# Optimization experiments

Measured on AMD Instinct MI355X. Metric: run time of the kernel, lower is better.

The kernel has to match this reference:

```python
import jax, jax.numpy as jnp
import numpy as np

B, S, VDIM, EDIM, K = 8, 2048, 1024, 256, 8192


def setup_inputs() -> dict:
    key = jax.random.key(0)
    k1, k2, k3, k4 = jax.random.split(key, 4)
    values = jax.random.normal(k1, (B, S, VDIM), dtype=jnp.float32)
    # nn.Linear(value_dim, embed_dim): weight [EDIM, VDIM], bias [EDIM]
    lim = 1.0 / np.sqrt(VDIM)
    W = jax.random.uniform(k2, (EDIM, VDIM), dtype=jnp.float32, minval=-lim, maxval=lim)
    b = jax.random.uniform(k3, (EDIM,), dtype=jnp.float32, minval=-lim, maxval=lim)
    # nn.Embedding default init: N(0, 1)
    codebook = jax.random.normal(k4, (K, EDIM), dtype=jnp.float32)
    return {"values": values, "W": W, "b": b, "codebook": codebook}


def reference(values, W, b, codebook):
    # Linear projection: [B,S,VDIM] -> [B,S,EDIM]
    projected = jnp.einsum("bsv,ev->bse", values, W) + b
    flat = projected.reshape(-1, projected.shape[-1])  # [N, EDIM]
    # Squared Euclidean distances via expansion (argmin-equivalent to cdist)
    d2 = (
        jnp.sum(flat * flat, axis=-1, keepdims=True)
        - 2.0 * (flat @ codebook.T)
        + jnp.sum(codebook * codebook, axis=-1)
    )  # [N, K]
    phase_ids = jnp.argmin(d2, axis=-1).reshape(values.shape[:-1])  # [B, S]
    quantized = codebook[phase_ids]  # [B, S, EDIM]
    sg = jax.lax.stop_gradient
    commitment_loss = jnp.mean((projected - sg(quantized)) ** 2)
    codebook_loss = jnp.mean((sg(projected) - quantized) ** 2)
    vq_loss = codebook_loss + 0.25 * commitment_loss
    # straight-through estimator
    quantized_st = projected + sg(quantized - projected)
    return quantized_st, phase_ids, vq_loss
```

## Files before the change

kernel.cpp:

```cpp
#include <hip/hip_runtime.h>

typedef __attribute__((ext_vector_type(8))) short bf16x8;
typedef __attribute__((ext_vector_type(4))) float f32x4;
typedef unsigned int uint32;
typedef unsigned long long ull;

#define NR 16384
#define VD 1024
#define ED 256
#define KC 8192
#define NBUCK 16
#define DELTA 2.0f
#define VSHIFT 128.0f

__device__ __forceinline__ uint32 f2u(float f){ return __float_as_uint(f); }
__device__ __forceinline__ float u2f(uint32 u){ return __uint_as_float(u); }

__device__ __forceinline__ uint32 pkbf(float lo, float hi){
  uint32 a = __float_as_uint(lo); a += 0x7fffu + ((a >> 16) & 1u);
  uint32 b = __float_as_uint(hi); b += 0x7fffu + ((b >> 16) & 1u);
  return (a >> 16) | (b & 0xffff0000u);
}

#define GLOAD_LDS16(g, l) __builtin_amdgcn_global_load_lds( \
    (const __attribute__((address_space(1))) void*)(g),     \
    (__attribute__((address_space(3))) void*)(l), 16, 0, 0)
#define GLOAD_LDS4(g, l) __builtin_amdgcn_global_load_lds(  \
    (const __attribute__((address_space(1))) void*)(g),     \
    (__attribute__((address_space(3))) void*)(l), 4, 0, 0)

__global__ __launch_bounds__(256) void wconv_kernel(
    const float* __restrict__ W, ushort* __restrict__ Whi, ushort* __restrict__ Wlo)
{
  const int idx = (blockIdx.x * 256 + threadIdx.x) * 8;
  float4 a = *(const float4*)(W + idx);
  float4 b = *(const float4*)(W + idx + 4);
  uint32 h01 = (f2u(a.x) >> 16) | (f2u(a.y) & 0xffff0000u);
  uint32 h23 = (f2u(a.z) >> 16) | (f2u(a.w) & 0xffff0000u);
  uint32 h45 = (f2u(b.x) >> 16) | (f2u(b.y) & 0xffff0000u);
  uint32 h67 = (f2u(b.z) >> 16) | (f2u(b.w) & 0xffff0000u);
  float r0 = a.x - u2f(f2u(a.x) & 0xffff0000u);
  float r1 = a.y - u2f(f2u(a.y) & 0xffff0000u);
  float r2 = a.z - u2f(f2u(a.z) & 0xffff0000u);
  float r3 = a.w - u2f(f2u(a.w) & 0xffff0000u);
  float r4 = b.x - u2f(f2u(b.x) & 0xffff0000u);
  float r5 = b.y - u2f(f2u(b.y) & 0xffff0000u);
  float r6 = b.z - u2f(f2u(b.z) & 0xffff0000u);
  float r7 = b.w - u2f(f2u(b.w) & 0xffff0000u);
  *(uint4*)(Whi + idx) = make_uint4(h01, h23, h45, h67);
  *(uint4*)(Wlo + idx) = make_uint4(pkbf(r0,r1), pkbf(r2,r3), pkbf(r4,r5), pkbf(r6,r7));
}

__global__ __launch_bounds__(512) void proj_mfma(
    const float* __restrict__ V, const ushort* __restrict__ WhiG,
    const ushort* __restrict__ WloG, const float* __restrict__ bias,
    float* __restrict__ C, ushort* __restrict__ Pbf)
{
  __shared__ __align__(16) char lds[128 * 132 * 4];
  const int rowbase = blockIdx.x * 128;
  const int colbase = blockIdx.y * 128;
  const int t = threadIdx.x, l = t & 63, w = t >> 6;
  const int c0 = l & 15, g = l >> 4;
  const int rg = w >> 2, cg = w & 3;

  const int srow = t >> 2, sq = t & 3;
  const float* aSrc = V + (size_t)(rowbase + srow) * VD + sq * 8;
  const int wu0 = (sq - (srow >> 3)) & 3;
  const ushort* whSrc = WhiG + (size_t)(colbase + srow) * VD + wu0 * 8;
  const ushort* wlSrc = WloG + (size_t)(colbase + srow) * VD + wu0 * 8;
  const int awOff = srow * 64 + (((sq + (srow >> 3)) & 3) << 4);
  char* wdst = lds + 16384 + (size_t)w * 1024;

  float4 bv[2];
  bv[0] = *(const float4*)&bias[colbase + cg * 32 + g * 4];
  bv[1] = *(const float4*)&bias[colbase + cg * 32 + 16 + g * 4];

  int vOff[4], wOff[2];
  #pragma unroll
  for (int bi = 0; bi < 4; ++bi) {
    int r = rg * 64 + bi * 16 + c0;
    vOff[bi] = r * 64 + (((g + (r >> 3)) & 3) << 4);
  }
  #pragma unroll
  for (int aj = 0; aj < 2; ++aj) {
    int r = cg * 32 + aj * 16 + c0;
    wOff[aj] = r * 64 + (((g + (r >> 3)) & 3) << 4);
  }

  f32x4 acc[2][4];
  #pragma unroll
  for (int aj = 0; aj < 2; ++aj)
    #pragma unroll
    for (int bi = 0; bi < 4; ++bi) acc[aj][bi] = (f32x4){0.f,0.f,0.f,0.f};

  float4 fa0, fa1;
  #define LOAD_A(ch)  { fa0 = *(const float4*)(aSrc + (ch) * 32); \
                        fa1 = *(const float4*)(aSrc + (ch) * 32 + 4); }
  #define STAGE_W(ch, buf) { \
    GLOAD_LDS16(whSrc + (ch) * 32, wdst + (buf) * 32768);        \
    GLOAD_LDS16(wlSrc + (ch) * 32, wdst + (buf) * 32768 + 8192); }
  #define CONV_WRITE(buf) { \
    uint32 h01 = (f2u(fa0.x)>>16)|(f2u(fa0.y)&0xffff0000u); \
    uint32 h23 = (f2u(fa0.z)>>16)|(f2u(fa0.w)&0xffff0000u); \
    uint32 h45 = (f2u(fa1.x)>>16)|(f2u(fa1.y)&0xffff0000u); \
    uint32 h67 = (f2u(fa1.z)>>16)|(f2u(fa1.w)&0xffff0000u); \
    float r0 = fa0.x - u2f(f2u(fa0.x)&0xffff0000u); \
    float r1 = fa0.y - u2f(f2u(fa0.y)&0xffff0000u); \
    float r2 = fa0.z - u2f(f2u(fa0.z)&0xffff0000u); \
    float r3 = fa0.w - u2f(f2u(fa0.w)&0xffff0000u); \
    float r4 = fa1.x - u2f(f2u(fa1.x)&0xffff0000u); \
    float r5 = fa1.y - u2f(f2u(fa1.y)&0xffff0000u); \
    float r6 = fa1.z - u2f(f2u(fa1.z)&0xffff0000u); \
    float r7 = fa1.w - u2f(f2u(fa1.w)&0xffff0000u); \
    *(uint4*)(lds + (buf)*32768 + awOff) = make_uint4(h01,h23,h45,h67); \
    *(uint4*)(lds + (buf)*32768 + 8192 + awOff) = \
        make_uint4(pkbf(r0,r1), pkbf(r2,r3), pkbf(r4,r5), pkbf(r6,r7)); }
  #define COMPUTE(buf) { \
    const char* Bq = lds + (buf) * 32768; \
    bf16x8 vh[4], vl[4], wh[2], wl[2]; \
    _Pragma("unroll") \
    for (int bi = 0; bi < 4; ++bi) { \
      vh[bi] = *(const bf16x8*)(Bq + vOff[bi]); \
      vl[bi] = *(const bf16x8*)(Bq + 8192 + vOff[bi]); } \
    _Pragma("unroll") \
    for (int aj = 0; aj < 2; ++aj) { \
      wh[aj] = *(const bf16x8*)(Bq + 16384 + wOff[aj]); \
      wl[aj] = *(const bf16x8*)(Bq + 24576 + wOff[aj]); } \
    _Pragma("unroll") \
    for (int aj = 0; aj < 2; ++aj) \
      _Pragma("unroll") \
      for (int bi = 0; bi < 4; ++bi) { \
        acc[aj][bi] = __builtin_amdgcn_mfma_f32_16x16x32_bf16(wh[aj], vh[bi], acc[aj][bi], 0, 0, 0); \
        acc[aj][bi] = __builtin_amdgcn_mfma_f32_16x16x32_bf16(wh[aj], vl[bi], acc[aj][bi], 0, 0, 0); \
        acc[aj][bi] = __builtin_amdgcn_mfma_f32_16x16x32_bf16(wl[aj], vh[bi], acc[aj][bi], 0, 0, 0); } }

  LOAD_A(0); STAGE_W(0, 0);
  CONV_WRITE(0);
  __syncthreads();
  int buf = 0;
  for (int ch = 0; ch < 32; ++ch) {
    if (ch < 31) { LOAD_A(ch + 1); STAGE_W(ch + 1, buf ^ 1); }
    COMPUTE(buf);
    if (ch < 31) CONV_WRITE(buf ^ 1);
    __syncthreads();
    buf ^= 1;
  }
  #undef LOAD_A
  #undef STAGE_W
  #undef CONV_WRITE
  #undef COMPUTE

  float* Cs = (float*)lds;
  #pragma unroll
  for (int aj = 0; aj < 2; ++aj)
    #pragma unroll
    for (int bi = 0; bi < 4; ++bi) {
      int prow = rg * 64 + bi * 16 + c0;
      int pcol = cg * 32 + aj * 16 + g * 4;
      f32x4 v = acc[aj][bi];
      float4 o = make_float4(v[0] + bv[aj].x, v[1] + bv[aj].y,
                             v[2] + bv[aj].z, v[3] + bv[aj].w);
      *(float4*)&Cs[prow * 132 + pcol] = o;
    }
  __syncthreads();
  {
    const int row = t >> 2, qd = t & 3;
    const float* src = &Cs[row * 132 + qd * 32];
    float* cdst = &C[(size_t)(rowbase + row) * ED + colbase + qd * 32];
    float4 vv[8];
    #pragma unroll
    for (int i = 0; i < 8; ++i) vv[i] = *(const float4*)(src + i * 4);
    #pragma unroll
    for (int i = 0; i < 8; ++i) *(float4*)(cdst + i * 4) = vv[i];
    uint4 pk[4];
    #pragma unroll
    for (int i = 0; i < 4; ++i)
      pk[i] = make_uint4(pkbf(vv[2*i].x, vv[2*i].y), pkbf(vv[2*i].z, vv[2*i].w),
                         pkbf(vv[2*i+1].x, vv[2*i+1].y), pkbf(vv[2*i+1].z, vv[2*i+1].w));
    uint4* pdst = (uint4*)&Pbf[(size_t)(rowbase + row) * ED + colbase + qd * 32];
    #pragma unroll
    for (int i = 0; i < 4; ++i) pdst[i] = pk[i];
  }
}

__global__ __launch_bounds__(256) void cnormbf_kernel(
    const float* __restrict__ CB, float* __restrict__ cnorm,
    float* __restrict__ cnAdj, ushort* __restrict__ CBbf)
{
  const int t = threadIdx.x, lane = t & 63, w = t >> 6;
  const int code = blockIdx.x * 4 + w;
  float4 c = *(const float4*)&CB[(size_t)code * ED + lane * 4];
  uint2 pk = make_uint2(pkbf(-2.f * c.x, -2.f * c.y), pkbf(-2.f * c.z, -2.f * c.w));
  *(uint2*)&CBbf[(size_t)code * ED + lane * 4] = pk;
  double s = (double)c.x * c.x + (double)c.y * c.y + (double)c.z * c.z + (double)c.w * c.w;
  #pragma unroll
  for (int off = 32; off; off >>= 1) s += __shfl_down(s, off, 64);
  if (lane == 0) {
    cnorm[code] = (float)s;
    cnAdj[code] = (float)s + VSHIFT;
  }
}

__global__ __launch_bounds__(512, 4) void mfma_dist(
    const ushort* __restrict__ CBbf, const ushort* __restrict__ Pbf,
    const float* __restrict__ cnAdj, uint4* __restrict__ top2s)
{
  __shared__ uint4 Tile[4096];
  __shared__ __align__(16) float cnL[2][64];
  __shared__ ull msh[128][2][2];

  const int bx = blockIdx.x;
  const int h = bx & 3;
  const int rowbase = (bx >> 2) * 128;
  const int cq0 = h * 2048;
  const int t = threadIdx.x, l = t & 63, w = t >> 6;
  const int rg = w >> 1, cg = w & 1;
  const int c0 = l & 15, g = l >> 4;

  {
    const ushort* gb = Pbf + ((size_t)rowbase << 8);
    #pragma unroll
    for (int i = 0; i < 8; ++i) {
      int lin = i * 8192 + t * 16;
      int crow = lin >> 9;
      int u = (lin >> 4) & 31;
      GLOAD_LDS16(gb + ((size_t)crow << 8) + (((u - crow) & 31) << 3),
                  (char*)Tile + lin);
    }
  }
  __syncthreads();
  bf16x8 breg[2][8];
  {
    const char* Tb = (const char*)Tile;
    #pragma unroll
    for (int rj = 0; rj < 2; ++rj) {
      const int row = rg * 32 + rj * 16 + c0;
      #pragma unroll
      for (int kk = 0; kk < 8; ++kk)
        breg[rj][kk] = *(const bf16x8*)(Tb + row * 512 + (((kk * 4 + g + row) & 31) << 4));
    }
  }
  __syncthreads();

  const int cl0 = cg * 32 + c0;
  const int cl1 = cg * 32 + 16 + c0;
  const int ab0 = cl0 * 512;
  const int ab1 = cl1 * 512;
  const int cc0 = cg * 32 + g * 4;
  const int cc1 = cg * 32 + 16 + g * 4;

  ull k1[2] = {~0ull, ~0ull};
  ull k2[2] = {~0ull, ~0ull};

  const ushort* sp[4]; int ldsoff[4];
  #pragma unroll
  for (int i = 0; i < 4; ++i) {
    int lin = i * 8192 + t * 16;
    int crow = lin >> 9;
    int u = (lin >> 4) & 31;
    sp[i] = CBbf + (((size_t)(cq0 + crow)) << 8) + (((u - crow) & 31) << 3);
    ldsoff[i] = lin;
  }
  const float* cnp = cnAdj + cq0 + l;

  #define STAGE(buf)                                                      \
    { char* db = (char*)Tile + (buf) * 32768;                             \
      _Pragma("unroll")                                                   \
      for (int i = 0; i < 4; ++i) {                                       \
        GLOAD_LDS16(sp[i], db + ldsoff[i]);                               \
        sp[i] += 16384;                                                   \
      }                                                                   \
      if (w == 0) GLOAD_LDS4(cnp, (char*)&cnL[buf][0]);                   \
      cnp += 64; }

  STAGE(0);
  __syncthreads();
  for (int ch = 0; ch < 32; ++ch) {
    const int buf = ch & 1;
    if (ch < 31) STAGE(buf ^ 1);
    f32x4 cn0 = *(const f32x4*)&cnL[buf][cc0];
    f32x4 cn1 = *(const f32x4*)&cnL[buf][cc1];
    f32x4 acc[2][2];
    acc[0][0] = cn0; acc[0][1] = cn0;
    acc[1][0] = cn1; acc[1][1] = cn1;
    {
      const char* Tb = (const char*)Tile + buf * 32768;
      int u0 = (g + cl0) & 31;
      int u1 = (g + cl1) & 31;
      #pragma unroll
      for (int kk = 0; kk < 8; ++kk) {
        bf16x8 a0 = *(const bf16x8*)(Tb + ab0 + (u0 << 4));
        bf16x8 a1 = *(const bf16x8*)(Tb + ab1 + (u1 << 4));
        u0 = (u0 + 4) & 31;
        u1 = (u1 + 4) & 31;
        #pragma unroll
        for (int rj = 0; rj < 2; ++rj) {
          acc[0][rj] = __builtin_amdgcn_mfma_f32_16x16x32_bf16(a0, breg[rj][kk], acc[0][rj], 0, 0, 0);
          acc[1][rj] = __builtin_amdgcn_mfma_f32_16x16x32_bf16(a1, breg[rj][kk], acc[1][rj], 0, 0, 0);
        }
      }
    }
    #pragma unroll
    for (int ci = 0; ci < 2; ++ci) {
      const int cbase = cq0 + ch * 64 + cg * 32 + ci * 16 + g * 4;
      #pragma unroll
      for (int rj = 0; rj < 2; ++rj)
        #pragma unroll
        for (int q = 0; q < 4; ++q) {
          ull key = ((ull)f2u(acc[ci][rj][q]) << 32) | (ull)(cbase + q);
          ull mx = k1[rj] > key ? k1[rj] : key;
          k1[rj] = k1[rj] < key ? k1[rj] : key;
          k2[rj] = k2[rj] < mx ? k2[rj] : mx;
        }
    }
    if ((ch & 7) == 7) {
      #pragma unroll
      for (int rj = 0; rj < 2; ++rj) {
        ull K1 = k1[rj], K2 = k2[rj];
        #pragma unroll
        for (int mask = 16; mask <= 32; mask <<= 1) {
          ull o1 = __shfl_xor(K1, mask);
          ull o2 = __shfl_xor(K2, mask);
          ull mx  = K1 > o1 ? K1 : o1;
          ull mn2 = K2 < o2 ? K2 : o2;
          K1 = K1 < o1 ? K1 : o1;
          K2 = mx < mn2 ? mx : mn2;
        }
        if (g == 0) {
          msh[rg * 32 + rj * 16 + c0][cg][0] = K1;
          msh[rg * 32 + rj * 16 + c0][cg][1] = K2;
        }
        k1[rj] = ~0ull; k2[rj] = ~0ull;
      }
      __syncthreads();
      if (t < 128) {
        ull a1 = msh[t][0][0], a2 = msh[t][0][1];
        ull b1 = msh[t][1][0], b2 = msh[t][1][1];
        ull K1  = a1 < b1 ? a1 : b1;
        ull mx  = a1 > b1 ? a1 : b1;
        ull mn2 = a2 < b2 ? a2 : b2;
        ull K2  = mx < mn2 ? mx : mn2;
        top2s[(size_t)(h * 4 + (ch >> 3)) * NR + rowbase + t] =
            make_uint4((uint32)(K1 >> 32), (uint32)K1, (uint32)(K2 >> 32), (uint32)K2);
      }
    }
    __syncthreads();
  }
  #undef STAGE
}

__global__ __launch_bounds__(256) void rescore_kernel(
    const uint4* __restrict__ top2s, const float* __restrict__ P,
    const float* __restrict__ CBF, const float* __restrict__ cnorm,
    int* __restrict__ ids, float* __restrict__ out_ids)
{
  const int t = threadIdx.x, l = t & 63, w = t >> 6;
  const int row = blockIdx.x * 4 + w;
  float m1 = 3.4e38f, m2 = 3.4e38f;
  uint32 i1 = 0, i2 = 0;
  if (l < NBUCK) {
    uint4 e = top2s[(size_t)l * NR + row];
    m1 = u2f(e.x); i1 = e.y & 8191u;
    m2 = u2f(e.z); i2 = e.w & 8191u;
  }
  float rm = m1;
  #pragma unroll
  for (int mask = 1; mask < 64; mask <<= 1) rm = fminf(rm, __shfl_xor(rm, mask));
  const float thr = rm + DELTA;
  ull qm1 = __ballot(l < NBUCK && m1 <= thr);
  ull qm2 = __ballot(l < NBUCK && m2 <= thr);
  float4 p = *(const float4*)&P[(size_t)row * ED + l * 4];
  double bd = 1e300; int bi = 0x7fffffff;
  #pragma unroll
  for (int cand = 0; cand < 2; ++cand) {
    ull qm = cand ? qm2 : qm1;
    uint32 myi = cand ? i2 : i1;
    while (qm) {
      int b = __ffsll(qm) - 1; qm &= qm - 1;
      int idx = __shfl((int)myi, b);
      const float4 c = *(const float4*)&CBF[(size_t)idx * ED + l * 4];
      double s = (double)p.x * c.x + (double)p.y * c.y + (double)p.z * c.z + (double)p.w * c.w;
      #pragma unroll
      for (int mask = 1; mask < 64; mask <<= 1) s += __shfl_xor(s, mask);
      double d2 = (double)cnorm[idx] - 2.0 * s;
      if (d2 < bd || (d2 == bd && idx < bi)) { bd = d2; bi = idx; }
    }
  }
  if (l == 0) {
    ids[row] = bi;
    out_ids[row] = (float)bi;
  }
}

__global__ __launch_bounds__(256) void gather_loss(
    const float* __restrict__ P, const float* __restrict__ CB,
    const int* __restrict__ ids, float* __restrict__ outq,
    float* __restrict__ loss)
{
  const int t = threadIdx.x, lane = t & 63, w = t >> 6;
  const int row = blockIdx.x * 4 + w;
  const int id = ids[row];
  float4 q = *(const float4*)&CB[(size_t)id * ED + lane * 4];
  float4 p = *(const float4*)&P[(size_t)row * ED + lane * 4];
  *(float4*)&outq[(size_t)row * ED + lane * 4] = q;
  float dx = p.x - q.x, dy = p.y - q.y, dz = p.z - q.z, dw = p.w - q.w;
  float s = dx * dx + dy * dy + dz * dz + dw * dw;
  #pragma unroll
  for (int off = 32; off; off >>= 1) s += __shfl_down(s, off, 64);
  __shared__ float partial[4];
  if (lane == 0) partial[w] = s;
  __syncthreads();
  if (t == 0){
    float tot = partial[0] + partial[1] + partial[2] + partial[3];
    atomicAdd(loss, tot * (1.25f / ((float)NR * (float)ED)));
  }
}

extern "C" void kernel_launch(void* const* d_in, const int* in_sizes, int n_in,
                              void* d_out, int out_size, void* d_ws, size_t ws_size,
                              hipStream_t stream) {
    const float* values = (const float*)d_in[0];
    const float* W      = (const float*)d_in[1];
    const float* bias   = (const float*)d_in[2];
    const float* CB     = (const float*)d_in[3];

    float* out      = (float*)d_out;
    float* out_q    = out;
    float* out_ids  = out + (size_t)NR * ED;
    float* out_loss = out_ids + NR;

    uint4*  top2s = (uint4*)out_q;
    ushort* Pbf   = (ushort*)(out_q + (size_t)NBUCK * NR * 4);

    float*  proj  = (float*)d_ws;
    float*  cnorm = proj + (size_t)NR * ED;
    float*  cnAdj = cnorm + KC;
    ushort* CBbf  = (ushort*)(cnAdj + KC);
    int*    ids   = (int*)(CBbf + (size_t)KC * ED);
    ushort* Whi   = (ushort*)(ids + NR);
    ushort* Wlo   = Whi + (size_t)ED * VD;

    hipMemsetAsync(out_loss, 0, sizeof(float), stream);
    wconv_kernel<<<ED * VD / (256 * 8), 256, 0, stream>>>(W, Whi, Wlo);
    cnormbf_kernel<<<KC / 4, 256, 0, stream>>>(CB, cnorm, cnAdj, CBbf);
    proj_mfma<<<dim3(NR / 128, ED / 128), 512, 0, stream>>>(values, Whi, Wlo, bias, proj, Pbf);
    mfma_dist<<<512, 512, 0, stream>>>(CBbf, Pbf, cnAdj, top2s);
    rescore_kernel<<<NR / 4, 256, 0, stream>>>(top2s, proj, CB, cnorm, ids, out_ids);
    gather_loss<<<NR / 4, 256, 0, stream>>>(proj, CB, ids, out_q, out_loss);
}
```

Before: 217.6 us.

## Halve mfma_dist row tile to 64 rows and double grid size

The distance kernel's tile shrinks from 128 to 64 projected rows per block and from 64 to 32 codes per chunk. Each wave now runs one MFMA accumulator instead of a 2x2 register block, and the grid grows from 512 to 1024 blocks. LDS and register use drop, which should raise occupancy and fill the CUs better. In exchange, register-level data reuse falls and codebook tiles are re-streamed twice as often with more barriers per code.

```diff
diff --git a/kernel.cpp b/kernel.cpp
--- a/kernel.cpp
+++ b/kernel.cpp
@@ -205,13 +205,13 @@
     const ushort* __restrict__ CBbf, const ushort* __restrict__ Pbf,
     const float* __restrict__ cnAdj, uint4* __restrict__ top2s)
 {
-  __shared__ uint4 Tile[4096];
+  __shared__ uint4 Tile[2048];
   __shared__ __align__(16) float cnL[2][64];
-  __shared__ ull msh[128][2][2];
+  __shared__ ull msh[64][2][2];
 
   const int bx = blockIdx.x;
   const int h = bx & 3;
-  const int rowbase = (bx >> 2) * 128;
+  const int rowbase = (bx >> 2) * 64;
   const int cq0 = h * 2048;
   const int t = threadIdx.x, l = t & 63, w = t >> 6;
   const int rg = w >> 1, cg = w & 1;
@@ -220,7 +220,7 @@
   {
     const ushort* gb = Pbf + ((size_t)rowbase << 8);
     #pragma unroll
-    for (int i = 0; i < 8; ++i) {
+    for (int i = 0; i < 4; ++i) {
       int lin = i * 8192 + t * 16;
       int crow = lin >> 9;
       int u = (lin >> 4) & 31;
@@ -229,124 +229,113 @@
     }
   }
   __syncthreads();
-  bf16x8 breg[2][8];
+  bf16x8 breg[8];
   {
     const char* Tb = (const char*)Tile;
-    #pragma unroll
-    for (int rj = 0; rj < 2; ++rj) {
-      const int row = rg * 32 + rj * 16 + c0;
-      #pragma unroll
-      for (int kk = 0; kk < 8; ++kk)
-        breg[rj][kk] = *(const bf16x8*)(Tb + row * 512 + (((kk * 4 + g + row) & 31) << 4));
-    }
-  }
-  __syncthreads();
-
-  const int cl0 = cg * 32 + c0;
-  const int cl1 = cg * 32 + 16 + c0;
+    const int prow = rg * 16 + c0;
+    #pragma unroll
+    for (int kk = 0; kk < 8; ++kk)
+      breg[kk] = *(const bf16x8*)(Tb + prow * 512 + (((kk * 4 + g + prow) & 31) << 4));
+  }
+  __syncthreads();
+
+  const int cl0 = cg * 16 + c0;
   const int ab0 = cl0 * 512;
-  const int ab1 = cl1 * 512;
-  const int cc0 = cg * 32 + g * 4;
-  const int cc1 = cg * 32 + 16 + g * 4;
-
-  ull k1[2] = {~0ull, ~0ull};
-  ull k2[2] = {~0ull, ~0ull};
-
-  const ushort* sp[4]; int ldsoff[4];
-  #pragma unroll
-  for (int i = 0; i < 4; ++i) {
-    int lin = i * 8192 + t * 16;
+  ull k1 = ~0ull, k2 = ~0ull;
+
+  const ushort* sp0; const ushort* sp1; int lo0, lo1;
+  {
+    int lin = t * 16;
     int crow = lin >> 9;
     int u = (lin >> 4) & 31;
-    sp[i] = CBbf + (((size_t)(cq0 + crow)) << 8) + (((u - crow) & 31) << 3);
-    ldsoff[i] = lin;
+    sp0 = CBbf + (((size_t)(cq0 + crow)) << 8) + (((u - crow) & 31) << 3);
+    lo0 = lin;
+    lin = 8192 + t * 16;
+    crow = lin >> 9;
+    u = (lin >> 4) & 31;
+    sp1 = CBbf + (((size_t)(cq0 + crow)) << 8) + (((u - crow) & 31) << 3);
+    lo1 = lin;
   }
   const float* cnp = cnAdj + cq0 + l;
 
-  #define STAGE(buf)                                                      \
-    { char* db = (char*)Tile + (buf) * 32768;                             \
-      _Pragma("unroll")                                                   \
-      for (int i = 0; i < 4; ++i) {                                       \
-        GLOAD_LDS16(sp[i], db + ldsoff[i]);                               \
-        sp[i] += 16384;                                                   \
-      }                                                                   \
-      if (w == 0) GLOAD_LDS4(cnp, (char*)&cnL[buf][0]);                   \
-      cnp += 64; }
-
-  STAGE(0);
-  __syncthreads();
-  for (int ch = 0; ch < 32; ++ch) {
-    const int buf = ch & 1;
-    if (ch < 31) STAGE(buf ^ 1);
-    f32x4 cn0 = *(const f32x4*)&cnL[buf][cc0];
-    f32x4 cn1 = *(const f32x4*)&cnL[buf][cc1];
-    f32x4 acc[2][2];
-    acc[0][0] = cn0; acc[0][1] = cn0;
-    acc[1][0] = cn1; acc[1][1] = cn1;
-    {
-      const char* Tb = (const char*)Tile + buf * 32768;
-      int u0 = (g + cl0) & 31;
-      int u1 = (g + cl1) & 31;
-      #pragma unroll
-      for (int kk = 0; kk < 8; ++kk) {
-        bf16x8 a0 = *(const bf16x8*)(Tb + ab0 + (u0 << 4));
-        bf16x8 a1 = *(const bf16x8*)(Tb + ab1 + (u1 << 4));
-        u0 = (u0 + 4) & 31;
-        u1 = (u1 + 4) & 31;
-        #pragma unroll
-        for (int rj = 0; rj < 2; ++rj) {
-          acc[0][rj] = __builtin_amdgcn_mfma_f32_16x16x32_bf16(a0, breg[rj][kk], acc[0][rj], 0, 0, 0);
-          acc[1][rj] = __builtin_amdgcn_mfma_f32_16x16x32_bf16(a1, breg[rj][kk], acc[1][rj], 0, 0, 0);
-        }
-      }
-    }
-    #pragma unroll
-    for (int ci = 0; ci < 2; ++ci) {
-      const int cbase = cq0 + ch * 64 + cg * 32 + ci * 16 + g * 4;
-      #pragma unroll
-      for (int rj = 0; rj < 2; ++rj)
-        #pragma unroll
-        for (int q = 0; q < 4; ++q) {
-          ull key = ((ull)f2u(acc[ci][rj][q]) << 32) | (ull)(cbase + q);
-          ull mx = k1[rj] > key ? k1[rj] : key;
-          k1[rj] = k1[rj] < key ? k1[rj] : key;
-          k2[rj] = k2[rj] < mx ? k2[rj] : mx;
-        }
-    }
-    if ((ch & 7) == 7) {
-      #pragma unroll
-      for (int rj = 0; rj < 2; ++rj) {
-        ull K1 = k1[rj], K2 = k2[rj];
-        #pragma unroll
-        for (int mask = 16; mask <= 32; mask <<= 1) {
-          ull o1 = __shfl_xor(K1, mask);
-          ull o2 = __shfl_xor(K2, mask);
-          ull mx  = K1 > o1 ? K1 : o1;
-          ull mn2 = K2 < o2 ? K2 : o2;
-          K1 = K1 < o1 ? K1 : o1;
-          K2 = mx < mn2 ? mx : mn2;
-        }
-        if (g == 0) {
-          msh[rg * 32 + rj * 16 + c0][cg][0] = K1;
-          msh[rg * 32 + rj * 16 + c0][cg][1] = K2;
-        }
-        k1[rj] = ~0ull; k2[rj] = ~0ull;
-      }
-      __syncthreads();
-      if (t < 128) {
-        ull a1 = msh[t][0][0], a2 = msh[t][0][1];
-        ull b1 = msh[t][1][0], b2 = msh[t][1][1];
-        ull K1  = a1 < b1 ? a1 : b1;
-        ull mx  = a1 > b1 ? a1 : b1;
-        ull mn2 = a2 < b2 ? a2 : b2;
-        ull K2  = mx < mn2 ? mx : mn2;
-        top2s[(size_t)(h * 4 + (ch >> 3)) * NR + rowbase + t] =
-            make_uint4((uint32)(K1 >> 32), (uint32)K1, (uint32)(K2 >> 32), (uint32)K2);
-      }
-    }
-    __syncthreads();
-  }
-  #undef STAGE
+  {
+    char* db = (char*)Tile;
+    GLOAD_LDS16(sp0, db + lo0); sp0 += 8192;
+    GLOAD_LDS16(sp1, db + lo1); sp1 += 8192;
+    if (w == 0) GLOAD_LDS4(cnp, (char*)&cnL[0][0]);
+    cnp += 64;
+  }
+  __syncthreads();
+
+  #define BODY(bufc, ch, SCN)                                              \
+  {                                                                        \
+    if ((ch) < 63) {                                                       \
+      char* db = (char*)Tile + ((bufc) ^ 1) * 16384;                       \
+      GLOAD_LDS16(sp0, db + lo0); sp0 += 8192;                             \
+      GLOAD_LDS16(sp1, db + lo1); sp1 += 8192;                             \
+      if (SCN) {                                                           \
+        if (w == 0) GLOAD_LDS4(cnp, (char*)&cnL[(((ch) + 1) >> 1) & 1][0]);\
+        cnp += 64;                                                         \
+      }                                                                    \
+    }                                                                      \
+    f32x4 acc = *(const f32x4*)&cnL[((ch) >> 1) & 1][((ch) & 1) * 32 + cg * 16 + g * 4]; \
+    {                                                                      \
+      const char* Tb = (const char*)Tile + (bufc) * 16384;                 \
+      int u0 = (g + cl0) & 31;                                             \
+      _Pragma("unroll")                                                    \
+      for (int kk = 0; kk < 8; ++kk) {                                     \
+        bf16x8 a0 = *(const bf16x8*)(Tb + ab0 + (u0 << 4));                \
+        u0 = (u0 + 4) & 31;                                                \
+        acc = __builtin_amdgcn_mfma_f32_16x16x32_bf16(a0, breg[kk], acc, 0, 0, 0); \
+      }                                                                    \
+    }                                                                      \
+    {                                                                      \
+      const int cbase = cq0 + (ch) * 32 + cg * 16 + g * 4;                 \
+      _Pragma("unroll")                                                    \
+      for (int q = 0; q < 4; ++q) {                                        \
+        ull key = ((ull)f2u(acc[q]) << 32) | (ull)(cbase + q);             \
+        ull mx = k1 > key ? k1 : key;                                      \
+        k1 = k1 < key ? k1 : key;                                          \
+        k2 = k2 < mx ? k2 : mx;                                            \
+      }                                                                    \
+    }                                                                      \
+    if (((ch) & 15) == 15) {                                               \
+      ull K1 = k1, K2 = k2;                                                \
+      _Pragma("unroll")                                                    \
+      for (int mask = 16; mask <= 32; mask <<= 1) {                        \
+        ull o1 = __shfl_xor(K1, mask);                                     \
+        ull o2 = __shfl_xor(K2, mask);                                     \
+        ull mxq = K1 > o1 ? K1 : o1;                                       \
+        ull mn2 = K2 < o2 ? K2 : o2;                                       \
+        K1 = K1 < o1 ? K1 : o1;                                            \
+        K2 = mxq < mn2 ? mxq : mn2;                                        \
+      }                                                                    \
+      if (g == 0) {                                                        \
+        msh[rg * 16 + c0][cg][0] = K1;                                     \
+        msh[rg * 16 + c0][cg][1] = K2;                                     \
+      }                                                                    \
+      k1 = ~0ull; k2 = ~0ull;                                              \
+      __syncthreads();                                                     \
+      if (t < 64) {                                                        \
+        ull a1 = msh[t][0][0], a2 = msh[t][0][1];                          \
+        ull b1 = msh[t][1][0], b2 = msh[t][1][1];                          \
+        ull K1f = a1 < b1 ? a1 : b1;                                       \
+        ull mxf = a1 > b1 ? a1 : b1;                                       \
+        ull mn2f = a2 < b2 ? a2 : b2;                                      \
+        ull K2f = mxf < mn2f ? mxf : mn2f;                                 \
+        top2s[(size_t)(h * 4 + ((ch) >> 4)) * NR + rowbase + t] =          \
+            make_uint4((uint32)(K1f >> 32), (uint32)K1f,                   \
+                       (uint32)(K2f >> 32), (uint32)K2f);                  \
+      }                                                                    \
+    }                                                                      \
+    __syncthreads();                                                       \
+  }
+
+  for (int ch = 0; ch < 64; ch += 2) {
+    BODY(0, ch, 0);
+    BODY(1, ch + 1, 1);
+  }
+  #undef BODY
 }
 
 __global__ __launch_bounds__(256) void rescore_kernel(
@@ -444,7 +433,7 @@
     wconv_kernel<<<ED * VD / (256 * 8), 256, 0, stream>>>(W, Whi, Wlo);
     cnormbf_kernel<<<KC / 4, 256, 0, stream>>>(CB, cnorm, cnAdj, CBbf);
     proj_mfma<<<dim3(NR / 128, ED / 128), 512, 0, stream>>>(values, Whi, Wlo, bias, proj, Pbf);
-    mfma_dist<<<512, 512, 0, stream>>>(CBbf, Pbf, cnAdj, top2s);
+    mfma_dist<<<1024, 512, 0, stream>>>(CBbf, Pbf, cnAdj, top2s);
     rescore_kernel<<<NR / 4, 256, 0, stream>>>(top2s, proj, CB, cnorm, ids, out_ids);
     gather_loss<<<NR / 4, 256, 0, stream>>>(proj, CB, ids, out_q, out_loss);
 }
```

Result: slower. 234.5 us (+7.8%).
